# Performance work log

Hardware: AMD Instinct MI355X
Metric: run time of the kernel (lower is better)

## Reference

```python
import jax, jax.numpy as jnp
import numpy as np

G = 512        # graphs in batch
N_PER = 256    # nodes per graph (equal-size graphs)
D = 128        # embed_dim
E_PER = 4096   # edges per graph
KEEP = 0.5
K = int(np.ceil(KEEP * N_PER))  # 128 nodes kept per graph (PyG topk: ceil(ratio*n))
N = G * N_PER
E = G * E_PER


def setup_inputs() -> dict:
    key = jax.random.key(0)
    k1, k2, k3, k4, k5 = jax.random.split(key, 5)
    x = jax.random.normal(k1, (N, D), jnp.float32)
    offs = (jnp.arange(G, dtype=jnp.int32) * N_PER)[:, None]
    src = jax.random.randint(k2, (G, E_PER), 0, N_PER, dtype=jnp.int32) + offs
    dst = jax.random.randint(k3, (G, E_PER), 0, N_PER, dtype=jnp.int32) + offs
    edge_index = jnp.stack([src.reshape(-1), dst.reshape(-1)], axis=0)  # [2, E], within-graph edges
    graph_indicator = jnp.repeat(jnp.arange(G, dtype=jnp.int32), N_PER)  # [N]
    gcn_w = jax.random.normal(k4, (D, 1), jnp.float32) / np.sqrt(D)
    gcn_b = jnp.zeros((1,), jnp.float32)
    lin_w = jax.random.normal(k5, (2 * D, D), jnp.float32) / np.sqrt(2 * D)
    lin_b = jnp.zeros((D,), jnp.float32)
    return {"input_feature": x, "graph_indicator": graph_indicator, "edge_index": edge_index,
            "gcn_w": gcn_w, "gcn_b": gcn_b, "lin_w": lin_w, "lin_b": lin_b}


def gcn_conv(x, edge_index, w, b):
    # PyG GCNConv: add self-loops, symmetric normalization, aggregate at target (edge_index[1]).
    n = x.shape[0]
    loop = jnp.arange(n, dtype=edge_index.dtype)
    row = jnp.concatenate([edge_index[0], loop])  # source
    col = jnp.concatenate([edge_index[1], loop])  # target
    deg = jax.ops.segment_sum(jnp.ones_like(col, dtype=x.dtype), col, num_segments=n)
    dinv = jax.lax.rsqrt(deg)  # deg >= 1 due to self-loops
    norm = dinv[row] * dinv[col]            # [E+N]
    xw = x @ w                              # [N, out]
    msg = xw[row] * norm[:, None]           # gather + scale
    agg = jax.ops.segment_sum(msg, col, num_segments=n)
    return agg + b


def reference(input_feature, graph_indicator, edge_index, gcn_w, gcn_b, lin_w, lin_b):
    # SAGPool: attention scores via GCNConv(d -> 1)
    score = gcn_conv(input_feature, edge_index, gcn_w, gcn_b).squeeze(-1)  # [N]
    # per-graph top-k mask (equal-size graphs -> reshape)
    s = score.reshape(G, N_PER)
    _, idx = jax.lax.top_k(s, K)                                          # [G, K]
    mask = jnp.zeros((G, N_PER), bool).at[jnp.arange(G)[:, None], idx].set(True)
    # gated features of kept nodes: x[mask] * tanh(score[mask])
    feat = (input_feature * jnp.tanh(score)[:, None]).reshape(G, N_PER, D)
    m = mask[..., None]
    # global mean/max pool over kept nodes per graph (exactly K kept per graph)
    mean = jnp.sum(jnp.where(m, feat, 0.0), axis=1) / K                   # [G, D]
    mx = jnp.max(jnp.where(m, feat, -jnp.inf), axis=1)                    # [G, D]
    readout = jnp.concatenate([mean, mx], axis=1)                         # [G, 2D]
    return readout @ lin_w + lin_b                                        # [G, D]
```

## Files before the change

### kernel.cpp

```cpp
#include <hip/hip_runtime.h>
#include <math.h>

#define NG   512
#define NPER 256
#define DD   128
#define EPER 4096
#define KK   128

__global__ __launch_bounds__(256, 2) void sag_fused(
    const float* __restrict__ x,
    const int*   __restrict__ esrc,
    const int*   __restrict__ edst,
    const float* __restrict__ gcn_w,
    const float* __restrict__ gcn_b,
    const float* __restrict__ lin_w,
    const float* __restrict__ lin_b,
    float* __restrict__ out)
{
  const int g    = blockIdx.x;
  const int tid  = threadIdx.x;
  const int lane = tid & 63;
  const int wave = tid >> 6;

  __shared__ float sW[DD];
  __shared__ float sXW[NPER];
  __shared__ float sScore[NPER];
  __shared__ float sDinv[NPER];
  __shared__ int   sDeg[NPER];
  __shared__ float sGate[NPER];
  __shared__ int   sKeep[NPER];
  __shared__ float sPartS[4][DD];
  __shared__ float sPartM[4][DD];
  __shared__ float sR[2 * DD];

  if (tid < DD) sW[tid] = gcn_w[tid];
  sDeg[tid] = 1;
  __syncthreads();

  const float*  xg  = x + (size_t)g * NPER * DD;
  const float4* xg4 = (const float4*)xg;
  const int j  = lane & 7;
  const int gr = lane >> 3;
  float wr[16];
  #pragma unroll
  for (int k = 0; k < 16; ++k) wr[k] = sW[j * 16 + k];

  #pragma unroll
  for (int i = 0; i < 8; ++i) {
    int node = wave * 64 + i * 8 + gr;
    const float4* p = xg4 + node * 32 + j * 4;
    float4 q0 = p[0], q1 = p[1], q2 = p[2], q3 = p[3];
    float acc = q0.x * wr[0]  + q0.y * wr[1]  + q0.z * wr[2]  + q0.w * wr[3]
              + q1.x * wr[4]  + q1.y * wr[5]  + q1.z * wr[6]  + q1.w * wr[7]
              + q2.x * wr[8]  + q2.y * wr[9]  + q2.z * wr[10] + q2.w * wr[11]
              + q3.x * wr[12] + q3.y * wr[13] + q3.z * wr[14] + q3.w * wr[15];
    acc += __shfl_xor(acc, 1);
    acc += __shfl_xor(acc, 2);
    acc += __shfl_xor(acc, 4);
    if (j == 0) sXW[node] = acc;
  }
  __syncthreads();

  const int* es = esrc + (size_t)g * EPER;
  const int* ed = edst + (size_t)g * EPER;
  for (int e = tid; e < EPER; e += 256) {
    atomicAdd(&sDeg[ed[e] & 255], 1);
  }
  __syncthreads();
  {
    float dv = 1.0f / sqrtf((float)sDeg[tid]);
    sDinv[tid]  = dv;
    sScore[tid] = sXW[tid] * dv * dv;
  }
  __syncthreads();

  for (int e = tid; e < EPER; e += 256) {
    int s = es[e] & 255;
    int d = ed[e] & 255;
    atomicAdd(&sScore[d], sXW[s] * sDinv[s] * sDinv[d]);
  }
  __syncthreads();

  const float bval = gcn_b[0];
  {
    float s_i = sScore[tid];
    sGate[tid] = tanhf(s_i + bval);
    int rank = 0;
    for (int jj = 0; jj < NPER; ++jj) {
      float s_j = sScore[jj];
      rank += (s_j > s_i) || (s_j == s_i && jj < tid);
    }
    sKeep[tid] = (rank < KK) ? 1 : 0;
  }
  __syncthreads();

  const float2* xg2 = (const float2*)xg;
  float sm0 = 0.f, sm1 = 0.f;
  float mx0 = -INFINITY, mx1 = -INFINITY;
  for (int n = 0; n < 64; ++n) {
    int node = wave * 64 + n;
    if (!sKeep[node]) continue;
    float gt = sGate[node];
    float2 p = xg2[node * 64 + lane];
    float a = p.x * gt;
    float b = p.y * gt;
    sm0 += a; sm1 += b;
    mx0 = fmaxf(mx0, a); mx1 = fmaxf(mx1, b);
  }
  sPartS[wave][lane * 2]     = sm0;
  sPartS[wave][lane * 2 + 1] = sm1;
  sPartM[wave][lane * 2]     = mx0;
  sPartM[wave][lane * 2 + 1] = mx1;
  __syncthreads();
  if (tid < DD) {
    float s = (sPartS[0][tid] + sPartS[1][tid]) + (sPartS[2][tid] + sPartS[3][tid]);
    float m = fmaxf(fmaxf(sPartM[0][tid], sPartM[1][tid]),
                    fmaxf(sPartM[2][tid], sPartM[3][tid]));
    sR[tid]      = s * (1.0f / KK);
    sR[DD + tid] = m;
  }
  __syncthreads();

  const float2* lw2 = (const float2*)lin_w;
  float a0 = 0.f, a1 = 0.f;
  #pragma unroll 4
  for (int kk = 0; kk < 64; ++kk) {
    int k = wave * 64 + kk;
    float rv = sR[k];
    float2 p = lw2[k * 64 + lane];
    a0 += rv * p.x;
    a1 += rv * p.y;
  }
  __syncthreads();
  sPartS[wave][lane * 2]     = a0;
  sPartS[wave][lane * 2 + 1] = a1;
  __syncthreads();
  if (tid < DD) {
    float o = (sPartS[0][tid] + sPartS[1][tid]) + (sPartS[2][tid] + sPartS[3][tid])
            + lin_b[tid];
    out[(size_t)g * DD + tid] = o;
  }
}

extern "C" void kernel_launch(void* const* d_in, const int* in_sizes, int n_in,
                              void* d_out, int out_size, void* d_ws, size_t ws_size,
                              hipStream_t stream) {
  const float* x  = (const float*)d_in[0];
  const int*   ei = (const int*)d_in[2];
  const float* gw = (const float*)d_in[3];
  const float* gb = (const float*)d_in[4];
  const float* lw = (const float*)d_in[5];
  const float* lb = (const float*)d_in[6];
  float* out = (float*)d_out;
  const int E = in_sizes[2] / 2;
  sag_fused<<<NG, 256, 0, stream>>>(x, ei, ei + E, gw, gb, lw, lb, out);
}
```

Before: 146.7 us.

## Use 1024-thread blocks per graph with compacted top-k gather and split rank counting

Raises the block size from 256 to 1024 threads so each graph's work is spread across 16 waves. Edge indices are prefetched as int4 at kernel start, and the rank computation is split four ways with shared atomics. Kept nodes are compacted into an index list so the pooling pass reads only the selected rows instead of branching over all nodes. The block-wide reductions are reorganised for 16 waves, and the extra waves may increase barrier and atomic contention.

```diff
diff --git a/kernel.cpp b/kernel.cpp
--- a/kernel.cpp
+++ b/kernel.cpp
@@ -6,8 +6,10 @@
 #define DD   128
 #define EPER 4096
 #define KK   128
+#define NT   1024
+#define NW   16
 
-__global__ __launch_bounds__(256, 2) void sag_fused(
+__global__ __launch_bounds__(NT, 4) void sag_fused(
     const float* __restrict__ x,
     const int*   __restrict__ esrc,
     const int*   __restrict__ edst,
@@ -22,123 +24,147 @@
   const int lane = tid & 63;
   const int wave = tid >> 6;
 
-  __shared__ float sW[DD];
-  __shared__ float sXW[NPER];
-  __shared__ float sScore[NPER];
-  __shared__ float sDinv[NPER];
-  __shared__ int   sDeg[NPER];
-  __shared__ float sGate[NPER];
-  __shared__ int   sKeep[NPER];
-  __shared__ float sPartS[4][DD];
-  __shared__ float sPartM[4][DD];
-  __shared__ float sR[2 * DD];
+  __shared__ float  sXW[NPER];
+  __shared__ float  sScore[NPER];
+  __shared__ float  sDinv[NPER];
+  __shared__ int    sDeg[NPER];
+  __shared__ int    sRank[NPER];
+  __shared__ int    sKept[KK];
+  __shared__ float  sGateK[KK];
+  __shared__ float2 sPS[NW][64];
+  __shared__ float2 sPM[NW][64];
+  __shared__ float2 sR2[DD];
 
-  if (tid < DD) sW[tid] = gcn_w[tid];
-  sDeg[tid] = 1;
+  const int4* es4 = (const int4*)(esrc + (size_t)g * EPER);
+  const int4* ed4 = (const int4*)(edst + (size_t)g * EPER);
+  int4 ev_s = es4[tid];
+  int4 ev_d = ed4[tid];
+
+  if (tid < NPER) { sDeg[tid] = 1; sRank[tid] = 0; }
   __syncthreads();
 
   const float*  xg  = x + (size_t)g * NPER * DD;
   const float4* xg4 = (const float4*)xg;
-  const int j  = lane & 7;
-  const int gr = lane >> 3;
-  float wr[16];
+  const int sl   = lane & 31;
+  const int half = lane >> 5;
+  float4 wr4 = ((const float4*)gcn_w)[sl];
   #pragma unroll
-  for (int k = 0; k < 16; ++k) wr[k] = sW[j * 16 + k];
-
-  #pragma unroll
-  for (int i = 0; i < 8; ++i) {
-    int node = wave * 64 + i * 8 + gr;
-    const float4* p = xg4 + node * 32 + j * 4;
-    float4 q0 = p[0], q1 = p[1], q2 = p[2], q3 = p[3];
-    float acc = q0.x * wr[0]  + q0.y * wr[1]  + q0.z * wr[2]  + q0.w * wr[3]
-              + q1.x * wr[4]  + q1.y * wr[5]  + q1.z * wr[6]  + q1.w * wr[7]
-              + q2.x * wr[8]  + q2.y * wr[9]  + q2.z * wr[10] + q2.w * wr[11]
-              + q3.x * wr[12] + q3.y * wr[13] + q3.z * wr[14] + q3.w * wr[15];
+  for (int r = 0; r < 8; ++r) {
+    int node = r * 32 + wave * 2 + half;
+    float4 q = xg4[node * 32 + sl];
+    float acc = q.x*wr4.x + q.y*wr4.y + q.z*wr4.z + q.w*wr4.w;
     acc += __shfl_xor(acc, 1);
     acc += __shfl_xor(acc, 2);
     acc += __shfl_xor(acc, 4);
-    if (j == 0) sXW[node] = acc;
+    acc += __shfl_xor(acc, 8);
+    acc += __shfl_xor(acc, 16);
+    if (sl == 0) sXW[node] = acc;
   }
+
+  atomicAdd(&sDeg[ev_d.x & 255], 1);
+  atomicAdd(&sDeg[ev_d.y & 255], 1);
+  atomicAdd(&sDeg[ev_d.z & 255], 1);
+  atomicAdd(&sDeg[ev_d.w & 255], 1);
   __syncthreads();
 
-  const int* es = esrc + (size_t)g * EPER;
-  const int* ed = edst + (size_t)g * EPER;
-  for (int e = tid; e < EPER; e += 256) {
-    atomicAdd(&sDeg[ed[e] & 255], 1);
-  }
-  __syncthreads();
-  {
+  if (tid < NPER) {
     float dv = 1.0f / sqrtf((float)sDeg[tid]);
     sDinv[tid]  = dv;
     sScore[tid] = sXW[tid] * dv * dv;
   }
   __syncthreads();
 
-  for (int e = tid; e < EPER; e += 256) {
-    int s = es[e] & 255;
-    int d = ed[e] & 255;
-    atomicAdd(&sScore[d], sXW[s] * sDinv[s] * sDinv[d]);
+  {
+    int s0 = ev_s.x & 255, d0 = ev_d.x & 255;
+    int s1 = ev_s.y & 255, d1 = ev_d.y & 255;
+    int s2 = ev_s.z & 255, d2 = ev_d.z & 255;
+    int s3 = ev_s.w & 255, d3 = ev_d.w & 255;
+    atomicAdd(&sScore[d0], sXW[s0] * sDinv[s0] * sDinv[d0]);
+    atomicAdd(&sScore[d1], sXW[s1] * sDinv[s1] * sDinv[d1]);
+    atomicAdd(&sScore[d2], sXW[s2] * sDinv[s2] * sDinv[d2]);
+    atomicAdd(&sScore[d3], sXW[s3] * sDinv[s3] * sDinv[d3]);
   }
   __syncthreads();
 
-  const float bval = gcn_b[0];
   {
-    float s_i = sScore[tid];
-    sGate[tid] = tanhf(s_i + bval);
-    int rank = 0;
-    for (int jj = 0; jj < NPER; ++jj) {
+    int node = tid & 255;
+    int seg  = tid >> 8;
+    float s_i = sScore[node];
+    int base = seg * 64;
+    int part = 0;
+    #pragma unroll 8
+    for (int jj = base; jj < base + 64; ++jj) {
       float s_j = sScore[jj];
-      rank += (s_j > s_i) || (s_j == s_i && jj < tid);
+      part += (s_j > s_i) || (s_j == s_i && jj < node);
     }
-    sKeep[tid] = (rank < KK) ? 1 : 0;
+    atomicAdd(&sRank[node], part);
+  }
+  __syncthreads();
+  {
+    const float bval = gcn_b[0];
+    if (tid < NPER) {
+      int r = sRank[tid];
+      if (r < KK) {
+        sKept[r]  = tid;
+        sGateK[r] = tanhf(sScore[tid] + bval);
+      }
+    }
   }
   __syncthreads();
 
   const float2* xg2 = (const float2*)xg;
-  float sm0 = 0.f, sm1 = 0.f;
-  float mx0 = -INFINITY, mx1 = -INFINITY;
-  for (int n = 0; n < 64; ++n) {
-    int node = wave * 64 + n;
-    if (!sKeep[node]) continue;
-    float gt = sGate[node];
+  float sm0 = 0.f, sm1 = 0.f, mx0 = -INFINITY, mx1 = -INFINITY;
+  #pragma unroll
+  for (int t = 0; t < 8; ++t) {
+    int kidx = wave * 8 + t;
+    int node = sKept[kidx];
+    float gt = sGateK[kidx];
     float2 p = xg2[node * 64 + lane];
-    float a = p.x * gt;
-    float b = p.y * gt;
+    float a = p.x * gt, b = p.y * gt;
     sm0 += a; sm1 += b;
     mx0 = fmaxf(mx0, a); mx1 = fmaxf(mx1, b);
   }
-  sPartS[wave][lane * 2]     = sm0;
-  sPartS[wave][lane * 2 + 1] = sm1;
-  sPartM[wave][lane * 2]     = mx0;
-  sPartM[wave][lane * 2 + 1] = mx1;
+  sPS[wave][lane] = make_float2(sm0, sm1);
+  sPM[wave][lane] = make_float2(mx0, mx1);
   __syncthreads();
-  if (tid < DD) {
-    float s = (sPartS[0][tid] + sPartS[1][tid]) + (sPartS[2][tid] + sPartS[3][tid]);
-    float m = fmaxf(fmaxf(sPartM[0][tid], sPartM[1][tid]),
-                    fmaxf(sPartM[2][tid], sPartM[3][tid]));
-    sR[tid]      = s * (1.0f / KK);
-    sR[DD + tid] = m;
+
+  if (wave == 0) {
+    float2 a = sPS[0][lane];
+    #pragma unroll
+    for (int w = 1; w < NW; ++w) { float2 p = sPS[w][lane]; a.x += p.x; a.y += p.y; }
+    sR2[lane] = make_float2(a.x * (1.0f / KK), a.y * (1.0f / KK));
+  } else if (wave == 1) {
+    float2 a = sPM[0][lane];
+    #pragma unroll
+    for (int w = 1; w < NW; ++w) {
+      float2 p = sPM[w][lane];
+      a.x = fmaxf(a.x, p.x); a.y = fmaxf(a.y, p.y);
+    }
+    sR2[64 + lane] = a;
   }
   __syncthreads();
 
+  const float*  sR  = (const float*)sR2;
   const float2* lw2 = (const float2*)lin_w;
   float a0 = 0.f, a1 = 0.f;
-  #pragma unroll 4
-  for (int kk = 0; kk < 64; ++kk) {
-    int k = wave * 64 + kk;
+  #pragma unroll
+  for (int t = 0; t < 16; ++t) {
+    int k = wave * 16 + t;
     float rv = sR[k];
     float2 p = lw2[k * 64 + lane];
     a0 += rv * p.x;
     a1 += rv * p.y;
   }
   __syncthreads();
-  sPartS[wave][lane * 2]     = a0;
-  sPartS[wave][lane * 2 + 1] = a1;
+  sPS[wave][lane] = make_float2(a0, a1);
   __syncthreads();
-  if (tid < DD) {
-    float o = (sPartS[0][tid] + sPartS[1][tid]) + (sPartS[2][tid] + sPartS[3][tid])
-            + lin_b[tid];
-    out[(size_t)g * DD + tid] = o;
+  if (wave == 0) {
+    float2 a = sPS[0][lane];
+    #pragma unroll
+    for (int w = 1; w < NW; ++w) { float2 p = sPS[w][lane]; a.x += p.x; a.y += p.y; }
+    float2 bb = ((const float2*)lin_b)[lane];
+    a.x += bb.x; a.y += bb.y;
+    ((float2*)out)[(size_t)g * 64 + lane] = a;
   }
 }
 
@@ -153,5 +179,5 @@
   const float* lb = (const float*)d_in[6];
   float* out = (float*)d_out;
   const int E = in_sizes[2] / 2;
-  sag_fused<<<NG, 256, 0, stream>>>(x, ei, ei + E, gw, gb, lw, lb, out);
+  sag_fused<<<NG, NT, 0, stream>>>(x, ei, ei + E, gw, gb, lw, lb, out);
 }
```

Measured after the change: 138.2 us. 5.8% less time.
